# Optimization experiments

Measured on AMD Instinct MI355X. Metric: run time of the kernel, lower is better.

Reference implementation:

```python
import jax, jax.numpy as jnp
import numpy as np

C = 1.0          # Poincare ball curvature
TEMP = 0.1       # softmax temperature
EPS = 1e-15
TANH_CLIP = 1.0 - 1e-5


def setup_inputs() -> dict:
    key = jax.random.key(0)
    ks = jax.random.split(key, 9)
    B, Din, H, D, P = 2048, 1024, 4096, 128, 1000
    inp = {
        "x": jax.random.normal(ks[0], (B, Din), dtype=jnp.float32),
        "W1": jax.random.normal(ks[1], (Din, H), dtype=jnp.float32) / np.sqrt(Din),
        "b1": jnp.zeros((H,), dtype=jnp.float32),
        "W2": jax.random.normal(ks[2], (H, H), dtype=jnp.float32) / np.sqrt(H),
        "b2": jnp.zeros((H,), dtype=jnp.float32),
        "W3": jax.random.normal(ks[3], (H, D), dtype=jnp.float32) / np.sqrt(H),
        "b3": jnp.zeros((D,), dtype=jnp.float32),
        # prototypes: points inside the unit ball (norm ~ 0.2)
        "prototypes": jax.random.normal(ks[4], (P, D), dtype=jnp.float32) * 0.02,
    }
    return inp


def _expmap0(u):
    sqc = np.sqrt(C)
    n = jnp.maximum(jnp.linalg.norm(u, axis=-1, keepdims=True), EPS)
    return jnp.tanh(sqc * n) * u / (sqc * n)


def _logmap0(y):
    sqc = np.sqrt(C)
    n = jnp.maximum(jnp.linalg.norm(y, axis=-1, keepdims=True), EPS)
    arg = jnp.clip(sqc * n, 0.0, TANH_CLIP)
    return jnp.arctanh(arg) * y / (sqc * n)


def _pairwise_dist(proto, xh):
    # dist(x=proto[P,D], y=xh[B,D]) = (2/sqrt(c)) * artanh(sqrt(c)*||(-x) (+) y||)
    # Mobius add norm computed from Gram products only (no [B,P,D] intermediate).
    # a = -proto, b = xh
    a2 = jnp.sum(proto * proto, axis=-1)          # [P]  ||a||^2
    b2 = jnp.sum(xh * xh, axis=-1)                # [B]  ||b||^2
    ab = -jnp.einsum('bd,pd->bp', xh, proto)      # [B,P] <a,b>
    a2_ = a2[None, :]
    b2_ = b2[:, None]
    alpha = 1.0 + 2.0 * C * ab + C * b2_
    beta = 1.0 - C * a2_
    gamma = 1.0 + 2.0 * C * ab + (C * C) * a2_ * b2_
    m2 = (alpha * alpha * a2_ + 2.0 * alpha * beta * ab + beta * beta * b2_) / (gamma * gamma)
    mnorm = jnp.sqrt(jnp.maximum(m2, 0.0))
    sqc = np.sqrt(C)
    arg = jnp.clip(sqc * mnorm, 0.0, TANH_CLIP)
    return (2.0 / sqc) * jnp.arctanh(arg)         # [B,P]


def reference(x, W1, b1, W2, b2, W3, b3, prototypes):
    h = jax.nn.gelu(x @ W1 + b1, approximate=False)
    h = jax.nn.gelu(h @ W2 + b2, approximate=False)
    u = h @ W3 + b3                               # [B,D]
    x_hyp = _expmap0(u)
    dists = _pairwise_dist(prototypes, x_hyp)     # [B,P]
    logits = -dists / TEMP
    pred = jnp.argmax(logits, axis=1)             # [B]
    pred_protos = jax.lax.stop_gradient(prototypes[pred])  # detach, as in torch
    feedback = _logmap0(pred_protos)              # [B,D]
    return logits, feedback
```

## Files before the change

### kernel.cpp

```cpp
#include <hip/hip_runtime.h>
#include <math.h>

#define B_SZ 2048
#define DIN  1024
#define H_SZ 4096
#define D_SZ 128
#define P_SZ 1000

typedef __attribute__((ext_vector_type(8))) short bf16x8;
typedef __attribute__((ext_vector_type(4))) float f32x4;

__device__ __forceinline__ float gelu_exact(float v) {
    return 0.5f * v * (1.0f + erff(v * 0.70710678118654752f));
}

__device__ __forceinline__ short f2bf(float f) {
    unsigned u = __float_as_uint(f);
    u = (u + 0x7fffu + ((u >> 16) & 1u)) >> 16;
    return (short)u;
}

__device__ __forceinline__ void gload_lds16(const void* g, void* l) {
    __builtin_amdgcn_global_load_lds(
        (__attribute__((address_space(1))) void*)(uintptr_t)g,
        (__attribute__((address_space(3))) void*)(uintptr_t)l,
        16, 0, 0);
}

__global__ __launch_bounds__(256) void cvt_bf16(
    const float* __restrict__ in, short* __restrict__ out, int n)
{
    const int i = (blockIdx.x * 256 + threadIdx.x) * 4;
    if (i + 3 < n) {
        const float4 v = *reinterpret_cast<const float4*>(&in[i]);
        short4 o;
        o.x = f2bf(v.x); o.y = f2bf(v.y); o.z = f2bf(v.z); o.w = f2bf(v.w);
        *reinterpret_cast<short4*>(&out[i]) = o;
    }
}

__global__ __launch_bounds__(256) void transpose_bf16(
    const float* __restrict__ W, short* __restrict__ WT, int K, int N)
{
    __shared__ float t[64][65];
    const int tid = threadIdx.x;
    const int tx = tid & 63, ty = tid >> 6;
    const int n0 = blockIdx.x * 64, k0 = blockIdx.y * 64;
    #pragma unroll
    for (int r = 0; r < 64; r += 4)
        t[r + ty][tx] = W[(size_t)(k0 + r + ty) * N + n0 + tx];
    __syncthreads();
    #pragma unroll
    for (int r = 0; r < 64; r += 4)
        WT[(size_t)(n0 + r + ty) * K + k0 + tx] = f2bf(t[tx][r + ty]);
}

__global__ __launch_bounds__(512) void gemm_big(
    const short* __restrict__ A, const short* __restrict__ BT,
    const float* __restrict__ bias, short* __restrict__ Cout,
    int M, int N, int K)
{
    extern __shared__ __align__(16) char smem[];

    const int tid  = threadIdx.x;
    const int lane = tid & 63;
    const int wid  = tid >> 6;
    const int row0 = blockIdx.y * 256;
    const int col0 = blockIdx.x * 128;
    const int wm = (wid >> 1) * 64;
    const int wn = (wid & 1) * 64;
    const int lr = lane & 15, kq = lane >> 4;

    const int NT = K >> 6;

    f32x4 acc[4][4];
    #pragma unroll
    for (int i = 0; i < 4; ++i)
        #pragma unroll
        for (int j = 0; j < 4; ++j) acc[i][j] = (f32x4){0.f, 0.f, 0.f, 0.f};

    const int srow = lane >> 3;
    const int kch  = (lane & 7) ^ srow;
    const short* Ag = A  + (size_t)(row0 + wid * 32 + srow) * K + kch * 8;
    const short* Bg = BT + (size_t)(col0 + wid * 16 + srow) * K + kch * 8;

    auto stage = [&](int t) {
        const int buf = t % 3;
        char* sA = smem + buf * 49152;
        char* sB = sA + 32768;
        const int k0 = t << 6;
        #pragma unroll
        for (int ii = 0; ii < 4; ++ii)
            gload_lds16(Ag + (size_t)ii * 8 * K + k0, sA + (wid * 4 + ii) * 1024);
        #pragma unroll
        for (int ii = 0; ii < 2; ++ii)
            gload_lds16(Bg + (size_t)ii * 8 * K + k0, sB + (wid * 2 + ii) * 1024);
    };

    stage(0);
    stage(1);
    asm volatile("s_waitcnt vmcnt(6)" ::: "memory");
    __builtin_amdgcn_s_barrier();
    asm volatile("" ::: "memory");

    for (int t = 0; t < NT; ++t) {
        const bool more = (t + 2) < NT;
        if (more) stage(t + 2);

        const char* sA = smem + (t % 3) * 49152;
        const char* sB = sA + 32768;

        #pragma unroll
        for (int ks = 0; ks < 2; ++ks) {
            bf16x8 af[4], bfv[4];
            #pragma unroll
            for (int i = 0; i < 4; ++i) {
                const int row = wm + i * 16 + lr;
                af[i] = *reinterpret_cast<const bf16x8*>(
                    sA + row * 128 + (((ks * 4 + kq) ^ (lr & 7)) * 16));
            }
            #pragma unroll
            for (int j = 0; j < 4; ++j) {
                const int row = wn + j * 16 + lr;
                bfv[j] = *reinterpret_cast<const bf16x8*>(
                    sB + row * 128 + (((ks * 4 + kq) ^ (lr & 7)) * 16));
            }
            __builtin_amdgcn_s_setprio(1);
            #pragma unroll
            for (int i = 0; i < 4; ++i)
                #pragma unroll
                for (int j = 0; j < 4; ++j)
                    acc[i][j] = __builtin_amdgcn_mfma_f32_16x16x32_bf16(
                        af[i], bfv[j], acc[i][j], 0, 0, 0);
            __builtin_amdgcn_s_setprio(0);
        }

        asm volatile("" ::: "memory");
        if (more) asm volatile("s_waitcnt vmcnt(6) lgkmcnt(0)" ::: "memory");
        else      asm volatile("s_waitcnt vmcnt(0) lgkmcnt(0)" ::: "memory");
        __builtin_amdgcn_s_barrier();
        asm volatile("" ::: "memory");
    }

    #pragma unroll
    for (int j = 0; j < 4; ++j) {
        const int col = col0 + wn + j * 16 + lr;
        const float bv = bias[col];
        #pragma unroll
        for (int i = 0; i < 4; ++i) {
            #pragma unroll
            for (int q = 0; q < 4; ++q) {
                const int row = row0 + wm + i * 16 + kq * 4 + q;
                float v = gelu_exact(acc[i][j][q] + bv);
                Cout[(size_t)row * N + col] = f2bf(v);
            }
        }
    }
}

__global__ __launch_bounds__(256) void gemm_small_splitk(
    const short* __restrict__ A, const short* __restrict__ BT,
    float* __restrict__ Cout, int M, int N, int K)
{
    __shared__ __align__(16) short sA[4 * 128 * 8];
    __shared__ __align__(16) short sB[4 * 128 * 8];

    const int tid  = threadIdx.x;
    const int lane = tid & 63;
    const int wid  = tid >> 6;
    const int row0 = blockIdx.y * 128;
    const int col0 = blockIdx.x * 128;
    const int wm = (wid >> 1) * 64;
    const int wn = (wid & 1) * 64;

    const int kpb    = K / gridDim.z;
    const int kstart = blockIdx.z * kpb;

    f32x4 acc[4][4];
    #pragma unroll
    for (int i = 0; i < 4; ++i)
        #pragma unroll
        for (int j = 0; j < 4; ++j) acc[i][j] = (f32x4){0.f, 0.f, 0.f, 0.f};

    const short* Ab = A  + (size_t)(row0 + lane) * K;
    const short* Bb = BT + (size_t)(col0 + lane) * K;
    short* ldsA = &sA[wid * (128 * 8)];
    short* ldsB = &sB[wid * (128 * 8)];

    const int kq = lane >> 4;
    const int lr = lane & 15;

    for (int k0 = kstart; k0 < kstart + kpb; k0 += 32) {
        gload_lds16(Ab + k0 + wid * 8,                  ldsA);
        gload_lds16(Ab + (size_t)64 * K + k0 + wid * 8, ldsA + 64 * 8);
        gload_lds16(Bb + k0 + wid * 8,                  ldsB);
        gload_lds16(Bb + (size_t)64 * K + k0 + wid * 8, ldsB + 64 * 8);
        __syncthreads();

        bf16x8 af[4], bfr[4];
        #pragma unroll
        for (int i = 0; i < 4; ++i)
            af[i] = *reinterpret_cast<const bf16x8*>(&sA[kq * (128 * 8) + (wm + i * 16 + lr) * 8]);
        #pragma unroll
        for (int j = 0; j < 4; ++j)
            bfr[j] = *reinterpret_cast<const bf16x8*>(&sB[kq * (128 * 8) + (wn + j * 16 + lr) * 8]);

        #pragma unroll
        for (int i = 0; i < 4; ++i)
            #pragma unroll
            for (int j = 0; j < 4; ++j)
                acc[i][j] = __builtin_amdgcn_mfma_f32_16x16x32_bf16(af[i], bfr[j], acc[i][j], 0, 0, 0);
        __syncthreads();
    }

    #pragma unroll
    for (int j = 0; j < 4; ++j) {
        const int col = col0 + wn + j * 16 + lr;
        if (col < N) {
            #pragma unroll
            for (int i = 0; i < 4; ++i)
                #pragma unroll
                for (int q = 0; q < 4; ++q) {
                    const int row = row0 + wm + i * 16 + kq * 4 + q;
                    atomicAdd(&Cout[(size_t)row * N + col], acc[i][j][q]);
                }
        }
    }
}

__global__ __launch_bounds__(128) void expmap_kernel(
    float* __restrict__ uxh, const float* __restrict__ b3, float* __restrict__ rowb2)
{
    const int b = blockIdx.x;
    const int d = threadIdx.x;
    float u = uxh[(size_t)b * D_SZ + d] + b3[d];

    float s = u * u;
    #pragma unroll
    for (int off = 32; off; off >>= 1) s += __shfl_down(s, off);
    __shared__ float part[2];
    if ((d & 63) == 0) part[d >> 6] = s;
    __syncthreads();
    const float n2 = part[0] + part[1];

    const float n = fmaxf(sqrtf(n2), 1e-15f);
    const float t = tanhf(n);
    uxh[(size_t)b * D_SZ + d] = u * (t / n);
    if (d == 0) rowb2[b] = t * t;
}

__global__ __launch_bounds__(128) void a2_kernel(
    const float* __restrict__ proto, float* __restrict__ a2g)
{
    const int p = blockIdx.x;
    const int d = threadIdx.x;
    const float y = proto[(size_t)p * D_SZ + d];
    float s = y * y;
    #pragma unroll
    for (int off = 32; off; off >>= 1) s += __shfl_down(s, off);
    __shared__ float part[2];
    if ((d & 63) == 0) part[d >> 6] = s;
    __syncthreads();
    if (d == 0) a2g[p] = part[0] + part[1];
}

__global__ __launch_bounds__(256) void dist_kernel(
    const float* __restrict__ xh, const float* __restrict__ proto,
    const float* __restrict__ rowb2, const float* __restrict__ a2g,
    float* __restrict__ logits)
{
    __shared__ float xs[128][68];
    __shared__ float ps[128][68];
    __shared__ float sb2[64], sa2[64];

    const int tid = threadIdx.x;
    const int pt = blockIdx.x * 64;
    const int bt = blockIdx.y * 64;

    #pragma unroll
    for (int r = 0; r < 8; ++r) {
        const int idx = r * 256 + tid;
        const int row = idx >> 5;
        const int dq  = (idx & 31) * 4;
        const float4 v = *reinterpret_cast<const float4*>(&xh[(size_t)(bt + row) * D_SZ + dq]);
        xs[dq + 0][row] = v.x; xs[dq + 1][row] = v.y; xs[dq + 2][row] = v.z; xs[dq + 3][row] = v.w;
        const int prow = pt + row;
        float4 w = {0.f, 0.f, 0.f, 0.f};
        if (prow < P_SZ) w = *reinterpret_cast<const float4*>(&proto[(size_t)prow * D_SZ + dq]);
        ps[dq + 0][row] = w.x; ps[dq + 1][row] = w.y; ps[dq + 2][row] = w.z; ps[dq + 3][row] = w.w;
    }
    if (tid < 64) {
        sb2[tid] = rowb2[bt + tid];
        sa2[tid] = (pt + tid < P_SZ) ? a2g[pt + tid] : 0.f;
    }
    __syncthreads();

    const int tx = tid & 15, ty = tid >> 4;
    float dot[4][4] = {};
    for (int d = 0; d < 128; ++d) {
        const float4 a4 = *reinterpret_cast<const float4*>(&xs[d][ty * 4]);
        const float4 b4 = *reinterpret_cast<const float4*>(&ps[d][tx * 4]);
        const float aa[4] = {a4.x, a4.y, a4.z, a4.w};
        const float bb[4] = {b4.x, b4.y, b4.z, b4.w};
        #pragma unroll
        for (int i = 0; i < 4; ++i)
            #pragma unroll
            for (int j = 0; j < 4; ++j)
                dot[i][j] = fmaf(aa[i], bb[j], dot[i][j]);
    }

    #pragma unroll
    for (int i = 0; i < 4; ++i) {
        const int b = bt + ty * 4 + i;
        const float b2 = sb2[ty * 4 + i];
        #pragma unroll
        for (int j = 0; j < 4; ++j) {
            const int p = pt + tx * 4 + j;
            if (p < P_SZ) {
                const float a2 = sa2[tx * 4 + j];
                const float ab = -dot[i][j];
                const float alpha = 1.f + 2.f * ab + b2;
                const float beta  = 1.f - a2;
                const float gamma = 1.f + 2.f * ab + a2 * b2;
                const float num = alpha * alpha * a2 + 2.f * alpha * beta * ab + beta * beta * b2;
                const float m2 = num / (gamma * gamma);
                const float mn = sqrtf(fmaxf(m2, 0.f));
                const float arg = fminf(mn, 0.99999f);
                const float dist = logf((1.f + arg) / (1.f - arg));
                logits[(size_t)b * P_SZ + p] = -10.f * dist;
            }
        }
    }
}

__global__ __launch_bounds__(256) void head_kernel(
    const float* __restrict__ logits, const float* __restrict__ proto,
    float* __restrict__ fb)
{
    const int b = blockIdx.x;
    const int tid = threadIdx.x;

    float best = -INFINITY; int bi = 0;
    for (int p = tid; p < P_SZ; p += 256) {
        const float v = logits[(size_t)b * P_SZ + p];
        if (v > best) { best = v; bi = p; }
    }
    __shared__ float bv[256];
    __shared__ int   bidx[256];
    bv[tid] = best; bidx[tid] = bi;
    __syncthreads();
    for (int s = 128; s; s >>= 1) {
        if (tid < s) {
            const float ov = bv[tid + s]; const int oi = bidx[tid + s];
            if (ov > bv[tid] || (ov == bv[tid] && oi < bidx[tid])) { bv[tid] = ov; bidx[tid] = oi; }
        }
        __syncthreads();
    }
    const int pred = bidx[0];
    __syncthreads();

    float y = 0.f;
    if (tid < 128) y = proto[(size_t)pred * D_SZ + tid];
    bv[tid] = y * y;
    __syncthreads();
    for (int s = 128; s; s >>= 1) {
        if (tid < s) bv[tid] += bv[tid + s];
        __syncthreads();
    }
    const float n2 = bv[0];
    if (tid < 128) {
        const float n = fmaxf(sqrtf(n2), 1e-15f);
        const float arg = fminf(n, 0.99999f);
        const float at = 0.5f * logf((1.f + arg) / (1.f - arg));
        fb[(size_t)b * D_SZ + tid] = at * (y / n);
    }
}

extern "C" void kernel_launch(void* const* d_in, const int* in_sizes, int n_in,
                              void* d_out, int out_size, void* d_ws, size_t ws_size,
                              hipStream_t stream)
{
    const float* x     = (const float*)d_in[0];
    const float* W1    = (const float*)d_in[1];
    const float* b1    = (const float*)d_in[2];
    const float* W2    = (const float*)d_in[3];
    const float* b2v   = (const float*)d_in[4];
    const float* W3    = (const float*)d_in[5];
    const float* b3    = (const float*)d_in[6];
    const float* proto = (const float*)d_in[7];

    float* logits = (float*)d_out;
    float* fb     = logits + (size_t)B_SZ * P_SZ;

    short* xb    = (short*)d_ws;
    short* w1t   = xb   + (size_t)B_SZ * DIN;
    short* w2t   = w1t  + (size_t)H_SZ * DIN;
    short* w3t   = w2t  + (size_t)H_SZ * H_SZ;
    short* h1    = w3t  + (size_t)D_SZ * H_SZ;
    short* h2    = h1   + (size_t)B_SZ * H_SZ;
    float* u     = (float*)(h2 + (size_t)B_SZ * H_SZ);
    float* rowb2 = u + (size_t)B_SZ * D_SZ;
    float* a2g   = rowb2 + B_SZ;

    static_cast<void>(hipFuncSetAttribute(
        reinterpret_cast<const void*>(&gemm_big),
        hipFuncAttributeMaxDynamicSharedMemorySize, 3 * 49152));

    cvt_bf16<<<(B_SZ * DIN) / 1024, 256, 0, stream>>>(x, xb, B_SZ * DIN);
    transpose_bf16<<<dim3(H_SZ / 64, DIN / 64), 256, 0, stream>>>(W1, w1t, DIN, H_SZ);
    transpose_bf16<<<dim3(H_SZ / 64, H_SZ / 64), 256, 0, stream>>>(W2, w2t, H_SZ, H_SZ);
    transpose_bf16<<<dim3(D_SZ / 64, H_SZ / 64), 256, 0, stream>>>(W3, w3t, H_SZ, D_SZ);

    gemm_big<<<dim3(H_SZ / 128, B_SZ / 256), 512, 3 * 49152, stream>>>(
        xb, w1t, b1, h1, B_SZ, H_SZ, DIN);
    gemm_big<<<dim3(H_SZ / 128, B_SZ / 256), 512, 3 * 49152, stream>>>(
        h1, w2t, b2v, h2, B_SZ, H_SZ, H_SZ);
    hipMemsetAsync(u, 0, (size_t)B_SZ * D_SZ * sizeof(float), stream);
    gemm_small_splitk<<<dim3(1, B_SZ / 128, 8), 256, 0, stream>>>(
        h2, w3t, u, B_SZ, D_SZ, H_SZ);

    expmap_kernel<<<B_SZ, 128, 0, stream>>>(u, b3, rowb2);
    a2_kernel<<<P_SZ, 128, 0, stream>>>(proto, a2g);
    dist_kernel<<<dim3((P_SZ + 63) / 64, B_SZ / 64), 256, 0, stream>>>(u, proto, rowb2, a2g, logits);
    head_kernel<<<B_SZ, 256, 0, stream>>>(logits, proto, fb);
}
```

Before: 301.3 us.

## Use MFMA for distance GEMM, split-K partial buffers for W3, vectorized transpose

Replaces the scalar FP32 dist kernel with a bf16 MFMA kernel that reads bf16 xh and prototypes from swizzled LDS. The third GEMM now reuses the pipelined gemm_big with a 16-way split-K, writing partial sums to a scratch buffer instead of using atomics and a memset, and expmap reduces those partials. The weight transpose uses float4 loads and 16-byte bf16 stores. These changes target the FP32 FMA-bound distance step and the atomic split-K, at the cost of bf16 rounding in the distances, which may change argmax ties.

```diff
diff --git a/kernel.cpp b/kernel.cpp
--- a/kernel.cpp
+++ b/kernel.cpp
@@ -6,6 +6,7 @@
 #define H_SZ 4096
 #define D_SZ 128
 #define P_SZ 1000
+#define PPAD 1024
 
 typedef __attribute__((ext_vector_type(8))) short bf16x8;
 typedef __attribute__((ext_vector_type(4))) float f32x4;
@@ -44,20 +45,51 @@
 {
     __shared__ float t[64][65];
     const int tid = threadIdx.x;
-    const int tx = tid & 63, ty = tid >> 6;
     const int n0 = blockIdx.x * 64, k0 = blockIdx.y * 64;
-    #pragma unroll
-    for (int r = 0; r < 64; r += 4)
-        t[r + ty][tx] = W[(size_t)(k0 + r + ty) * N + n0 + tx];
-    __syncthreads();
-    #pragma unroll
-    for (int r = 0; r < 64; r += 4)
-        WT[(size_t)(n0 + r + ty) * K + k0 + tx] = f2bf(t[tx][r + ty]);
-}
-
+
+    #pragma unroll
+    for (int i = 0; i < 4; ++i) {
+        const int idx = i * 256 + tid;
+        const int r  = idx >> 4;
+        const int c4 = (idx & 15) * 4;
+        const float4 v = *reinterpret_cast<const float4*>(&W[(size_t)(k0 + r) * N + n0 + c4]);
+        t[r][c4 + 0] = v.x; t[r][c4 + 1] = v.y; t[r][c4 + 2] = v.z; t[r][c4 + 3] = v.w;
+    }
+    __syncthreads();
+
+    #pragma unroll
+    for (int i = 0; i < 2; ++i) {
+        const int idx = i * 256 + tid;
+        const int n  = idx >> 3;
+        const int kc = (idx & 7) * 8;
+        bf16x8 o;
+        #pragma unroll
+        for (int q = 0; q < 8; ++q) o[q] = f2bf(t[kc + q][n]);
+        *reinterpret_cast<bf16x8*>(&WT[(size_t)(n0 + n) * K + k0 + kc]) = o;
+    }
+}
+
+__global__ __launch_bounds__(128) void proto_prep(
+    const float* __restrict__ proto, short* __restrict__ protob,
+    float* __restrict__ a2gp)
+{
+    const int p = blockIdx.x;
+    const int d = threadIdx.x;
+    const float y = (p < P_SZ) ? proto[(size_t)p * D_SZ + d] : 0.f;
+    protob[(size_t)p * D_SZ + d] = f2bf(y);
+    float s = y * y;
+    #pragma unroll
+    for (int off = 32; off; off >>= 1) s += __shfl_down(s, off);
+    __shared__ float part[2];
+    if ((d & 63) == 0) part[d >> 6] = s;
+    __syncthreads();
+    if (d == 0) a2gp[p] = part[0] + part[1];
+}
+
+template<int EPI>
 __global__ __launch_bounds__(512) void gemm_big(
     const short* __restrict__ A, const short* __restrict__ BT,
-    const float* __restrict__ bias, short* __restrict__ Cout,
+    const float* __restrict__ bias, void* __restrict__ Cout,
     int M, int N, int K)
 {
     extern __shared__ __align__(16) char smem[];
@@ -71,7 +103,9 @@
     const int wn = (wid & 1) * 64;
     const int lr = lane & 15, kq = lane >> 4;
 
-    const int NT = K >> 6;
+    const int kpb    = K / gridDim.z;
+    const int kstart = blockIdx.z * kpb;
+    const int NT = kpb >> 6;
 
     f32x4 acc[4][4];
     #pragma unroll
@@ -81,8 +115,8 @@
 
     const int srow = lane >> 3;
     const int kch  = (lane & 7) ^ srow;
-    const short* Ag = A  + (size_t)(row0 + wid * 32 + srow) * K + kch * 8;
-    const short* Bg = BT + (size_t)(col0 + wid * 16 + srow) * K + kch * 8;
+    const short* Ag = A  + (size_t)(row0 + wid * 32 + srow) * K + kstart + kch * 8;
+    const short* Bg = BT + (size_t)(col0 + wid * 16 + srow) * K + kstart + kch * 8;
 
     auto stage = [&](int t) {
         const int buf = t % 3;
@@ -145,95 +179,33 @@
     #pragma unroll
     for (int j = 0; j < 4; ++j) {
         const int col = col0 + wn + j * 16 + lr;
-        const float bv = bias[col];
+        const float bv = (EPI == 0) ? bias[col] : 0.f;
         #pragma unroll
         for (int i = 0; i < 4; ++i) {
             #pragma unroll
             for (int q = 0; q < 4; ++q) {
                 const int row = row0 + wm + i * 16 + kq * 4 + q;
-                float v = gelu_exact(acc[i][j][q] + bv);
-                Cout[(size_t)row * N + col] = f2bf(v);
+                if (EPI == 0) {
+                    float v = gelu_exact(acc[i][j][q] + bv);
+                    ((short*)Cout)[(size_t)row * N + col] = f2bf(v);
+                } else {
+                    ((float*)Cout)[((size_t)blockIdx.z * M + row) * N + col] = acc[i][j][q];
+                }
             }
         }
     }
 }
 
-__global__ __launch_bounds__(256) void gemm_small_splitk(
-    const short* __restrict__ A, const short* __restrict__ BT,
-    float* __restrict__ Cout, int M, int N, int K)
-{
-    __shared__ __align__(16) short sA[4 * 128 * 8];
-    __shared__ __align__(16) short sB[4 * 128 * 8];
-
-    const int tid  = threadIdx.x;
-    const int lane = tid & 63;
-    const int wid  = tid >> 6;
-    const int row0 = blockIdx.y * 128;
-    const int col0 = blockIdx.x * 128;
-    const int wm = (wid >> 1) * 64;
-    const int wn = (wid & 1) * 64;
-
-    const int kpb    = K / gridDim.z;
-    const int kstart = blockIdx.z * kpb;
-
-    f32x4 acc[4][4];
-    #pragma unroll
-    for (int i = 0; i < 4; ++i)
-        #pragma unroll
-        for (int j = 0; j < 4; ++j) acc[i][j] = (f32x4){0.f, 0.f, 0.f, 0.f};
-
-    const short* Ab = A  + (size_t)(row0 + lane) * K;
-    const short* Bb = BT + (size_t)(col0 + lane) * K;
-    short* ldsA = &sA[wid * (128 * 8)];
-    short* ldsB = &sB[wid * (128 * 8)];
-
-    const int kq = lane >> 4;
-    const int lr = lane & 15;
-
-    for (int k0 = kstart; k0 < kstart + kpb; k0 += 32) {
-        gload_lds16(Ab + k0 + wid * 8,                  ldsA);
-        gload_lds16(Ab + (size_t)64 * K + k0 + wid * 8, ldsA + 64 * 8);
-        gload_lds16(Bb + k0 + wid * 8,                  ldsB);
-        gload_lds16(Bb + (size_t)64 * K + k0 + wid * 8, ldsB + 64 * 8);
-        __syncthreads();
-
-        bf16x8 af[4], bfr[4];
-        #pragma unroll
-        for (int i = 0; i < 4; ++i)
-            af[i] = *reinterpret_cast<const bf16x8*>(&sA[kq * (128 * 8) + (wm + i * 16 + lr) * 8]);
-        #pragma unroll
-        for (int j = 0; j < 4; ++j)
-            bfr[j] = *reinterpret_cast<const bf16x8*>(&sB[kq * (128 * 8) + (wn + j * 16 + lr) * 8]);
-
-        #pragma unroll
-        for (int i = 0; i < 4; ++i)
-            #pragma unroll
-            for (int j = 0; j < 4; ++j)
-                acc[i][j] = __builtin_amdgcn_mfma_f32_16x16x32_bf16(af[i], bfr[j], acc[i][j], 0, 0, 0);
-        __syncthreads();
-    }
-
-    #pragma unroll
-    for (int j = 0; j < 4; ++j) {
-        const int col = col0 + wn + j * 16 + lr;
-        if (col < N) {
-            #pragma unroll
-            for (int i = 0; i < 4; ++i)
-                #pragma unroll
-                for (int q = 0; q < 4; ++q) {
-                    const int row = row0 + wm + i * 16 + kq * 4 + q;
-                    atomicAdd(&Cout[(size_t)row * N + col], acc[i][j][q]);
-                }
-        }
-    }
-}
-
 __global__ __launch_bounds__(128) void expmap_kernel(
-    float* __restrict__ uxh, const float* __restrict__ b3, float* __restrict__ rowb2)
+    const float* __restrict__ up, const float* __restrict__ b3,
+    short* __restrict__ xhb, float* __restrict__ rowb2)
 {
     const int b = blockIdx.x;
     const int d = threadIdx.x;
-    float u = uxh[(size_t)b * D_SZ + d] + b3[d];
+    float u = b3[d];
+    #pragma unroll
+    for (int z = 0; z < 16; ++z)
+        u += up[((size_t)z * B_SZ + b) * D_SZ + d];
 
     float s = u * u;
     #pragma unroll
@@ -245,89 +217,95 @@
 
     const float n = fmaxf(sqrtf(n2), 1e-15f);
     const float t = tanhf(n);
-    uxh[(size_t)b * D_SZ + d] = u * (t / n);
+    xhb[(size_t)b * D_SZ + d] = f2bf(u * (t / n));
     if (d == 0) rowb2[b] = t * t;
 }
 
-__global__ __launch_bounds__(128) void a2_kernel(
-    const float* __restrict__ proto, float* __restrict__ a2g)
-{
-    const int p = blockIdx.x;
-    const int d = threadIdx.x;
-    const float y = proto[(size_t)p * D_SZ + d];
-    float s = y * y;
-    #pragma unroll
-    for (int off = 32; off; off >>= 1) s += __shfl_down(s, off);
-    __shared__ float part[2];
-    if ((d & 63) == 0) part[d >> 6] = s;
-    __syncthreads();
-    if (d == 0) a2g[p] = part[0] + part[1];
-}
-
-__global__ __launch_bounds__(256) void dist_kernel(
-    const float* __restrict__ xh, const float* __restrict__ proto,
-    const float* __restrict__ rowb2, const float* __restrict__ a2g,
+__global__ __launch_bounds__(256) void dist_mfma(
+    const short* __restrict__ xhb, const short* __restrict__ protob,
+    const float* __restrict__ rowb2, const float* __restrict__ a2gp,
     float* __restrict__ logits)
 {
-    __shared__ float xs[128][68];
-    __shared__ float ps[128][68];
-    __shared__ float sb2[64], sa2[64];
-
-    const int tid = threadIdx.x;
+    __shared__ __align__(16) char xs[128 * 256];
+    __shared__ __align__(16) char ps[64 * 256];
+
+    const int tid  = threadIdx.x;
+    const int lane = tid & 63, wid = tid >> 6;
     const int pt = blockIdx.x * 64;
-    const int bt = blockIdx.y * 64;
-
-    #pragma unroll
-    for (int r = 0; r < 8; ++r) {
-        const int idx = r * 256 + tid;
-        const int row = idx >> 5;
-        const int dq  = (idx & 31) * 4;
-        const float4 v = *reinterpret_cast<const float4*>(&xh[(size_t)(bt + row) * D_SZ + dq]);
-        xs[dq + 0][row] = v.x; xs[dq + 1][row] = v.y; xs[dq + 2][row] = v.z; xs[dq + 3][row] = v.w;
-        const int prow = pt + row;
-        float4 w = {0.f, 0.f, 0.f, 0.f};
-        if (prow < P_SZ) w = *reinterpret_cast<const float4*>(&proto[(size_t)prow * D_SZ + dq]);
-        ps[dq + 0][row] = w.x; ps[dq + 1][row] = w.y; ps[dq + 2][row] = w.z; ps[dq + 3][row] = w.w;
-    }
-    if (tid < 64) {
-        sb2[tid] = rowb2[bt + tid];
-        sa2[tid] = (pt + tid < P_SZ) ? a2g[pt + tid] : 0.f;
-    }
-    __syncthreads();
-
-    const int tx = tid & 15, ty = tid >> 4;
-    float dot[4][4] = {};
-    for (int d = 0; d < 128; ++d) {
-        const float4 a4 = *reinterpret_cast<const float4*>(&xs[d][ty * 4]);
-        const float4 b4 = *reinterpret_cast<const float4*>(&ps[d][tx * 4]);
-        const float aa[4] = {a4.x, a4.y, a4.z, a4.w};
-        const float bb[4] = {b4.x, b4.y, b4.z, b4.w};
+    const int bt = blockIdx.y * 128;
+    const int wm = (wid >> 1) * 64;
+    const int wn = (wid & 1) * 32;
+    const int lr = lane & 15, kq = lane >> 4;
+
+    const int rl = lane >> 4, c = lane & 15;
+    #pragma unroll
+    for (int i = 0; i < 8; ++i) {
+        const int row = wid * 32 + i * 4 + rl;
+        const int lc  = (c & 8) | ((c & 7) ^ (row & 7));
+        gload_lds16(xhb + (size_t)(bt + row) * D_SZ + lc * 8,
+                    xs + (wid * 8 + i) * 1024);
+    }
+    #pragma unroll
+    for (int i = 0; i < 4; ++i) {
+        const int row = wid * 16 + i * 4 + rl;
+        const int lc  = (c & 8) | ((c & 7) ^ (row & 7));
+        gload_lds16(protob + (size_t)(pt + row) * D_SZ + lc * 8,
+                    ps + (wid * 4 + i) * 1024);
+    }
+    __syncthreads();
+
+    f32x4 acc[4][2];
+    #pragma unroll
+    for (int i = 0; i < 4; ++i)
+        #pragma unroll
+        for (int j = 0; j < 2; ++j) acc[i][j] = (f32x4){0.f, 0.f, 0.f, 0.f};
+
+    #pragma unroll
+    for (int ks = 0; ks < 4; ++ks) {
+        const int kslot = ks * 4 + kq;
+        bf16x8 af[4], bfv[2];
+        #pragma unroll
+        for (int i = 0; i < 4; ++i) {
+            const int row = wm + i * 16 + lr;
+            const int ph = (kslot & 8) | ((kslot & 7) ^ (row & 7));
+            af[i] = *reinterpret_cast<const bf16x8*>(xs + row * 256 + ph * 16);
+        }
+        #pragma unroll
+        for (int j = 0; j < 2; ++j) {
+            const int row = wn + j * 16 + lr;
+            const int ph = (kslot & 8) | ((kslot & 7) ^ (row & 7));
+            bfv[j] = *reinterpret_cast<const bf16x8*>(ps + row * 256 + ph * 16);
+        }
         #pragma unroll
         for (int i = 0; i < 4; ++i)
             #pragma unroll
-            for (int j = 0; j < 4; ++j)
-                dot[i][j] = fmaf(aa[i], bb[j], dot[i][j]);
-    }
-
-    #pragma unroll
-    for (int i = 0; i < 4; ++i) {
-        const int b = bt + ty * 4 + i;
-        const float b2 = sb2[ty * 4 + i];
-        #pragma unroll
-        for (int j = 0; j < 4; ++j) {
-            const int p = pt + tx * 4 + j;
-            if (p < P_SZ) {
-                const float a2 = sa2[tx * 4 + j];
-                const float ab = -dot[i][j];
-                const float alpha = 1.f + 2.f * ab + b2;
-                const float beta  = 1.f - a2;
-                const float gamma = 1.f + 2.f * ab + a2 * b2;
-                const float num = alpha * alpha * a2 + 2.f * alpha * beta * ab + beta * beta * b2;
-                const float m2 = num / (gamma * gamma);
-                const float mn = sqrtf(fmaxf(m2, 0.f));
-                const float arg = fminf(mn, 0.99999f);
-                const float dist = logf((1.f + arg) / (1.f - arg));
-                logits[(size_t)b * P_SZ + p] = -10.f * dist;
+            for (int j = 0; j < 2; ++j)
+                acc[i][j] = __builtin_amdgcn_mfma_f32_16x16x32_bf16(
+                    af[i], bfv[j], acc[i][j], 0, 0, 0);
+    }
+
+    #pragma unroll
+    for (int j = 0; j < 2; ++j) {
+        const int p = pt + wn + j * 16 + lr;
+        if (p < P_SZ) {
+            const float a2 = a2gp[p];
+            #pragma unroll
+            for (int i = 0; i < 4; ++i) {
+                #pragma unroll
+                for (int q = 0; q < 4; ++q) {
+                    const int b = bt + wm + i * 16 + kq * 4 + q;
+                    const float b2 = rowb2[b];
+                    const float ab = -acc[i][j][q];
+                    const float alpha = 1.f + 2.f * ab + b2;
+                    const float beta  = 1.f - a2;
+                    const float gamma = 1.f + 2.f * ab + a2 * b2;
+                    const float num = alpha * alpha * a2 + 2.f * alpha * beta * ab + beta * beta * b2;
+                    const float m2 = num / (gamma * gamma);
+                    const float mn = sqrtf(fmaxf(m2, 0.f));
+                    const float arg = fminf(mn, 0.99999f);
+                    const float dist = logf((1.f + arg) / (1.f - arg));
+                    logits[(size_t)b * P_SZ + p] = -10.f * dist;
+                }
             }
         }
     }
@@ -392,35 +370,40 @@
     float* logits = (float*)d_out;
     float* fb     = logits + (size_t)B_SZ * P_SZ;
 
-    short* xb    = (short*)d_ws;
-    short* w1t   = xb   + (size_t)B_SZ * DIN;
-    short* w2t   = w1t  + (size_t)H_SZ * DIN;
-    short* w3t   = w2t  + (size_t)H_SZ * H_SZ;
-    short* h1    = w3t  + (size_t)D_SZ * H_SZ;
-    short* h2    = h1   + (size_t)B_SZ * H_SZ;
-    float* u     = (float*)(h2 + (size_t)B_SZ * H_SZ);
-    float* rowb2 = u + (size_t)B_SZ * D_SZ;
-    float* a2g   = rowb2 + B_SZ;
+    short* xb     = (short*)d_ws;
+    short* w1t    = xb    + (size_t)B_SZ * DIN;
+    short* w2t    = w1t   + (size_t)H_SZ * DIN;
+    short* w3t    = w2t   + (size_t)H_SZ * H_SZ;
+    short* h1     = w3t   + (size_t)D_SZ * H_SZ;
+    short* h2     = h1    + (size_t)B_SZ * H_SZ;
+    short* xhb    = h2    + (size_t)B_SZ * H_SZ;
+    short* protob = xhb   + (size_t)B_SZ * D_SZ;
+    float* rowb2  = (float*)(protob + (size_t)PPAD * D_SZ);
+    float* a2gp   = rowb2 + B_SZ;
+    float* up     = (float*)h1;
 
     static_cast<void>(hipFuncSetAttribute(
-        reinterpret_cast<const void*>(&gemm_big),
+        reinterpret_cast<const void*>(&gemm_big<0>),
+        hipFuncAttributeMaxDynamicSharedMemorySize, 3 * 49152));
+    static_cast<void>(hipFuncSetAttribute(
+        reinterpret_cast<const void*>(&gemm_big<1>),
         hipFuncAttributeMaxDynamicSharedMemorySize, 3 * 49152));
 
     cvt_bf16<<<(B_SZ * DIN) / 1024, 256, 0, stream>>>(x, xb, B_SZ * DIN);
     transpose_bf16<<<dim3(H_SZ / 64, DIN / 64), 256, 0, stream>>>(W1, w1t, DIN, H_SZ);
     transpose_bf16<<<dim3(H_SZ / 64, H_SZ / 64), 256, 0, stream>>>(W2, w2t, H_SZ, H_SZ);
     transpose_bf16<<<dim3(D_SZ / 64, H_SZ / 64), 256, 0, stream>>>(W3, w3t, H_SZ, D_SZ);
-
-    gemm_big<<<dim3(H_SZ / 128, B_SZ / 256), 512, 3 * 49152, stream>>>(
+    proto_prep<<<PPAD, 128, 0, stream>>>(proto, protob, a2gp);
+
+    gemm_big<0><<<dim3(H_SZ / 128, B_SZ / 256), 512, 3 * 49152, stream>>>(
         xb, w1t, b1, h1, B_SZ, H_SZ, DIN);
-    gemm_big<<<dim3(H_SZ / 128, B_SZ / 256), 512, 3 * 49152, stream>>>(
+    gemm_big<0><<<dim3(H_SZ / 128, B_SZ / 256), 512, 3 * 49152, stream>>>(
         h1, w2t, b2v, h2, B_SZ, H_SZ, H_SZ);
-    hipMemsetAsync(u, 0, (size_t)B_SZ * D_SZ * sizeof(float), stream);
-    gemm_small_splitk<<<dim3(1, B_SZ / 128, 8), 256, 0, stream>>>(
-        h2, w3t, u, B_SZ, D_SZ, H_SZ);
-
-    expmap_kernel<<<B_SZ, 128, 0, stream>>>(u, b3, rowb2);
-    a2_kernel<<<P_SZ, 128, 0, stream>>>(proto, a2g);
-    dist_kernel<<<dim3((P_SZ + 63) / 64, B_SZ / 64), 256, 0, stream>>>(u, proto, rowb2, a2g, logits);
+    gemm_big<1><<<dim3(1, B_SZ / 256, 16), 512, 3 * 49152, stream>>>(
+        h2, w3t, nullptr, up, B_SZ, D_SZ, H_SZ);
+
+    expmap_kernel<<<B_SZ, 128, 0, stream>>>(up, b3, xhb, rowb2);
+    dist_mfma<<<dim3(PPAD / 64, B_SZ / 128), 256, 0, stream>>>(
+        xhb, protob, rowb2, a2gp, logits);
     head_kernel<<<B_SZ, 256, 0, stream>>>(logits, proto, fb);
 }
```

After: 272.0 us. 9.7% less time.
